# Optimization experiments

Hardware: AMD Instinct MI355X
Metric: run time of the kernel (lower is better)

The kernel has to match this reference:

```python
import jax, jax.numpy as jnp
import numpy as np

NUM_THETAS = 64   # bump_steps == num_thetas == 64
NUM_PTS = 100
B = 256           # number of graphs
N = B * NUM_PTS   # total nodes
SCALE = 500.0     # sigmoid sharpness used by EctLayer
HID = 4 * 1024


def _linear_init(key, fan_in, shape):
    s = 1.0 / np.sqrt(fan_in)
    return jax.random.uniform(key, shape, jnp.float32, -s, s)


def setup_inputs() -> dict:
    key = jax.random.key(0)
    ks = jax.random.split(key, 8)
    x = jax.random.normal(ks[0], (N, 2), jnp.float32)
    batch_idx = jnp.repeat(jnp.arange(B), NUM_PTS)  # [N] graph id per node
    t = jnp.linspace(0.0, 2.0 * np.pi, NUM_THETAS)
    V = jnp.stack([jnp.sin(t), jnp.cos(t)], axis=0)          # [2, T] directions
    lin = jnp.linspace(-1.0, 1.0, NUM_THETAS)                # [bump] thresholds
    d = NUM_THETAS * NUM_THETAS
    W1 = _linear_init(ks[1], d, (d, HID)); b1 = _linear_init(ks[2], d, (HID,))
    W2 = _linear_init(ks[3], HID, (HID, HID)); b2 = _linear_init(ks[4], HID, (HID,))
    W3 = _linear_init(ks[5], HID, (HID, 2 * NUM_PTS)); b3 = _linear_init(ks[6], HID, (2 * NUM_PTS,))
    return {"x": x, "batch_idx": batch_idx, "V": V, "lin": lin,
            "W1": W1, "b1": b1, "W2": W2, "b2": b2, "W3": W3, "b3": b3}


def ect_layer(x, idx, V, lin, num_graphs):
    # x: [N,2], V: [2,T] -> node heights nh: [N,T]
    nh = x @ V
    # soft-threshold binning: [N, bump, T]
    ecc = jax.nn.sigmoid(SCALE * (lin[None, :, None] - nh[:, None, :]))
    # per-graph scatter-sum over nodes -> [B, bump, T]
    e = jax.ops.segment_sum(ecc, idx, num_segments=num_graphs)
    # normalized=True: divide by per-graph max
    return e / jnp.amax(e, axis=(1, 2), keepdims=True)


def reference(x, batch_idx, V, lin, W1, b1, W2, b2, W3, b3):
    ect = ect_layer(x, batch_idx, V, lin, B)          # [B, 64, 64]
    h = ect.reshape(B, -1)                            # Flatten
    h = jnp.tanh(h @ W1 + b1)
    h = jnp.tanh(h @ W2 + b2)
    pts = (h @ W3 + b3).reshape(-1, 2)                # [B*NUM_PTS, 2]
    idx2 = jnp.repeat(jnp.arange(B), NUM_PTS)
    decoded = ect_layer(pts, idx2, V, lin, B)         # [B, 64, 64]
    return decoded, pts
```

## Files before the change

### kernel.cpp

```cpp
#include <hip/hip_runtime.h>
#include <hip/hip_bf16.h>

typedef short bf16x8 __attribute__((ext_vector_type(8)));
typedef short s16x4 __attribute__((ext_vector_type(4)));
typedef float f32x4 __attribute__((ext_vector_type(4)));
typedef unsigned u32x4 __attribute__((ext_vector_type(4)));

#define ECT_SCALE 500.0f

__device__ __forceinline__ bool detect_f32(const void* w) {
    const unsigned* p = (const unsigned*)w;
    int sane = 0;
#pragma unroll
    for (int i = 0; i < 16; i++) {
        unsigned e = (p[i] >> 7) & 0xFFu;
        sane += (e >= 100u && e <= 140u) ? 1 : 0;
    }
    return sane < 10;
}

__device__ __forceinline__ float ld_f(const void* p, int i, bool f32) {
    return f32 ? ((const float*)p)[i]
               : __bfloat162float(((const __hip_bfloat16*)p)[i]);
}

__device__ __forceinline__ void split_f(float v, short& hi, short& lo) {
    __hip_bfloat16 h = __float2bfloat16(v);
    hi = (short)__bfloat16_as_short(h);
    lo = (short)__bfloat16_as_short(__float2bfloat16(v - __bfloat162float(h)));
}

__device__ __forceinline__ float sig_fast(float x) {
    float t = __builtin_amdgcn_fmed3f(x, 0.0f, 1.0f);
    return t * t * (3.0f - 2.0f * t);
}

__global__ __launch_bounds__(512)
void ect1_kernel(const void* __restrict__ x, const void* __restrict__ V,
                 const void* __restrict__ lin, const void* __restrict__ sent,
                 short* __restrict__ eh, short* __restrict__ el)
{
    __shared__ float in_lds[200];
    __shared__ float nh[100 * 64];
    __shared__ float wmax[8];

    const bool f32 = detect_f32(sent);
    const int g = blockIdx.x, tid = threadIdx.x;
    const int t = tid & 63, wv = tid >> 6;

    if (tid < 200) in_lds[tid] = ld_f(x, g * 200 + tid, f32);
    const float sv = ld_f(V, t, f32);
    const float cv = ld_f(V, 64 + t, f32);
    float zs[8];
#pragma unroll
    for (int k = 0; k < 8; k++)
        zs[k] = (ECT_SCALE / 8.0f) * ld_f(lin, wv + 8 * k, f32) + 0.5f;
    __syncthreads();

    for (int n = wv; n < 100; n += 8)
        nh[n * 64 + t] = in_lds[2 * n] * sv + in_lds[2 * n + 1] * cv;

    float e[8];
#pragma unroll
    for (int k = 0; k < 8; k++) e[k] = 0.0f;
    __syncthreads();

    for (int n = 0; n < 100; n++) {
        const float ws = (ECT_SCALE / 8.0f) * nh[n * 64 + t];
#pragma unroll
        for (int k = 0; k < 8; k++)
            e[k] += sig_fast(zs[k] - ws);
    }

    float mx = e[0];
#pragma unroll
    for (int k = 1; k < 8; k++) mx = fmaxf(mx, e[k]);
#pragma unroll
    for (int off = 32; off > 0; off >>= 1)
        mx = fmaxf(mx, __shfl_xor(mx, off, 64));
    if (t == 0) wmax[wv] = mx;
    __syncthreads();
    float gm = wmax[0];
#pragma unroll
    for (int k = 1; k < 8; k++) gm = fmaxf(gm, wmax[k]);
    const float sc = 1.0f / gm;

#pragma unroll
    for (int k = 0; k < 8; k++) {
        short hi, lo;
        split_f(e[k] * sc, hi, lo);
        eh[g * 4096 + tid + 512 * k] = hi;
        el[g * 4096 + tid + 512 * k] = lo;
    }
}

#define GEMM_STAGE(K_, N_, GUARD_N)                                            \
    {                                                                          \
        _Pragma("unroll")                                                      \
        for (int i = 0; i < 2; i++) {                                          \
            int r = rr + 32 * i;                                               \
            *(bf16x8*)&Ahs[r][cc] =                                            \
                *(const bf16x8*)&Ah[(size_t)(bm * 64 + r) * K_ + k0 + cc];     \
            *(bf16x8*)&Als[r][cc] =                                            \
                *(const bf16x8*)&Al[(size_t)(bm * 64 + r) * K_ + k0 + cc];     \
        }                                                                      \
        {                                                                      \
            const int wn = lane;                                               \
            const int wk = wv * 16;                                            \
            const bool okn = !(GUARD_N) || (n0c + wn < N_);                    \
            unsigned hp[8], lp[8];                                             \
            if (f32) {                                                         \
                float w0[16];                                                  \
                _Pragma("unroll")                                              \
                for (int j = 0; j < 16; j++)                                   \
                    w0[j] = okn ? ((const float*)W)[(size_t)(k0 + wk + j) * N_ + n0c + wn] : 0.0f; \
                _Pragma("unroll")                                              \
                for (int jp = 0; jp < 8; jp++) {                               \
                    unsigned ua = __float_as_uint(w0[2 * jp]);                 \
                    unsigned ub = __float_as_uint(w0[2 * jp + 1]);             \
                    unsigned ha = ua & 0xFFFF0000u, hb = ub & 0xFFFF0000u;     \
                    hp[jp] = (ha >> 16) | hb;                                  \
                    float la = w0[2 * jp] - __uint_as_float(ha);               \
                    float lb = w0[2 * jp + 1] - __uint_as_float(hb);           \
                    lp[jp] = (__float_as_uint(la) >> 16) |                     \
                             (__float_as_uint(lb) & 0xFFFF0000u);              \
                }                                                              \
            } else {                                                           \
                unsigned short wu[16];                                         \
                _Pragma("unroll")                                              \
                for (int j = 0; j < 16; j++)                                   \
                    wu[j] = okn ? ((const unsigned short*)W)[(size_t)(k0 + wk + j) * N_ + n0c + wn] : (unsigned short)0; \
                _Pragma("unroll")                                              \
                for (int jp = 0; jp < 8; jp++) {                               \
                    hp[jp] = (unsigned)wu[2 * jp] | ((unsigned)wu[2 * jp + 1] << 16); \
                    lp[jp] = 0u;                                               \
                }                                                              \
            }                                                                  \
            *(u32x4*)&Bhs[wn][wk]     = (u32x4){hp[0], hp[1], hp[2], hp[3]};   \
            *(u32x4*)&Bhs[wn][wk + 8] = (u32x4){hp[4], hp[5], hp[6], hp[7]};   \
            *(u32x4*)&Bls[wn][wk]     = (u32x4){lp[0], lp[1], lp[2], lp[3]};   \
            *(u32x4*)&Bls[wn][wk + 8] = (u32x4){lp[4], lp[5], lp[6], lp[7]};   \
        }                                                                      \
        __syncthreads();                                                       \
        _Pragma("unroll")                                                      \
        for (int kh = 0; kh < 2; kh++) {                                       \
            bf16x8 ah[2], al[2], bh[2], bl[2];                                 \
            _Pragma("unroll")                                                  \
            for (int im = 0; im < 2; im++) {                                   \
                ah[im] = *(const bf16x8*)&Ahs[mrow0 + im * 16 + l16][kh * 32 + quad * 8]; \
                al[im] = *(const bf16x8*)&Als[mrow0 + im * 16 + l16][kh * 32 + quad * 8]; \
            }                                                                  \
            _Pragma("unroll")                                                  \
            for (int jn = 0; jn < 2; jn++) {                                   \
                bh[jn] = *(const bf16x8*)&Bhs[ncol0 + jn * 16 + l16][kh * 32 + quad * 8]; \
                bl[jn] = *(const bf16x8*)&Bls[ncol0 + jn * 16 + l16][kh * 32 + quad * 8]; \
            }                                                                  \
            _Pragma("unroll")                                                  \
            for (int im = 0; im < 2; im++)                                     \
                _Pragma("unroll")                                              \
                for (int jn = 0; jn < 2; jn++) {                               \
                    acc[im][jn] = __builtin_amdgcn_mfma_f32_16x16x32_bf16(ah[im], bh[jn], acc[im][jn], 0, 0, 0); \
                    acc[im][jn] = __builtin_amdgcn_mfma_f32_16x16x32_bf16(ah[im], bl[jn], acc[im][jn], 0, 0, 0); \
                    acc[im][jn] = __builtin_amdgcn_mfma_f32_16x16x32_bf16(al[im], bh[jn], acc[im][jn], 0, 0, 0); \
                }                                                              \
        }                                                                      \
        __syncthreads();                                                       \
    }

template<bool GUARD>
__global__ __launch_bounds__(256)
void gemm_sk(const short* __restrict__ Ah, const short* __restrict__ Al,
             const void* __restrict__ W, const void* __restrict__ sent,
             float* __restrict__ pre, int N_, int K_, int kzbits, int kiters)
{
    __shared__ short Ahs[64][72], Als[64][72], Bhs[64][72], Bls[64][72];
    const bool f32 = detect_f32(sent);
    const int bm = blockIdx.y;
    const int bn = blockIdx.x >> kzbits;
    const int kz = blockIdx.x & ((1 << kzbits) - 1);
    const int tid = threadIdx.x;
    const int wv = tid >> 6, lane = tid & 63, quad = lane >> 4, l16 = lane & 15;
    const int mrow0 = (wv & 1) * 32, ncol0 = (wv >> 1) * 32;
    const int rr = tid >> 3, cc = (tid & 7) * 8;
    const int n0c = bn * 64;

    f32x4 acc[2][2];
#pragma unroll
    for (int i = 0; i < 2; i++)
#pragma unroll
        for (int j = 0; j < 2; j++) acc[i][j] = (f32x4){0.f, 0.f, 0.f, 0.f};

    int k0 = kz * (kiters * 64);
    for (int it = 0; it < kiters; it++, k0 += 64)
        GEMM_STAGE(K_, N_, GUARD)

#pragma unroll
    for (int im = 0; im < 2; im++)
#pragma unroll
        for (int jn = 0; jn < 2; jn++) {
            const int n = n0c + ncol0 + jn * 16 + l16;
            if (!GUARD || n < N_) {
#pragma unroll
                for (int r = 0; r < 4; r++) {
                    const int m = bm * 64 + mrow0 + im * 16 + quad * 4 + r;
                    atomicAdd(&pre[(size_t)m * N_ + n], acc[im][jn][r]);
                }
            }
        }
}

__global__ __launch_bounds__(256)
void finalize_tanh(const float* __restrict__ pre, const void* __restrict__ bias,
                   const void* __restrict__ sent,
                   short* __restrict__ Oh, short* __restrict__ Ol)
{
    const bool f32 = detect_f32(sent);
    const int idx = (blockIdx.x * 256 + threadIdx.x) * 4;
    f32x4 v = *(const f32x4*)&pre[idx];
    const int n = idx & 4095;
    s16x4 hi, lo;
#pragma unroll
    for (int j = 0; j < 4; j++) {
        float t = v[j] + ld_f(bias, n + j, f32);
        t = 1.0f - 2.0f * __builtin_amdgcn_rcpf(1.0f + __expf(2.0f * t));
        short h, l;
        split_f(t, h, l);
        hi[j] = h; lo[j] = l;
    }
    *(s16x4*)&Oh[idx] = hi;
    *(s16x4*)&Ol[idx] = lo;
}

__global__ __launch_bounds__(512)
void ect2_kernel(const float* __restrict__ part, const void* __restrict__ bias3,
                 const void* __restrict__ V, const void* __restrict__ lin,
                 const void* __restrict__ sent,
                 float* __restrict__ dec, float* __restrict__ pts_out)
{
    __shared__ float in_lds[200];
    __shared__ float nh[100 * 64];
    __shared__ float wmax[8];

    const bool f32 = detect_f32(sent);
    const int g = blockIdx.x, tid = threadIdx.x;
    const int t = tid & 63, wv = tid >> 6;

    if (tid < 200) {
        float v = part[g * 200 + tid] + ld_f(bias3, tid, f32);
        in_lds[tid] = v;
        pts_out[g * 200 + tid] = v;
    }
    const float sv = ld_f(V, t, f32);
    const float cv = ld_f(V, 64 + t, f32);
    float zs[8];
#pragma unroll
    for (int k = 0; k < 8; k++)
        zs[k] = (ECT_SCALE / 8.0f) * ld_f(lin, wv + 8 * k, f32) + 0.5f;
    __syncthreads();

    for (int n = wv; n < 100; n += 8)
        nh[n * 64 + t] = in_lds[2 * n] * sv + in_lds[2 * n + 1] * cv;

    float e[8];
#pragma unroll
    for (int k = 0; k < 8; k++) e[k] = 0.0f;
    __syncthreads();

    for (int n = 0; n < 100; n++) {
        const float ws = (ECT_SCALE / 8.0f) * nh[n * 64 + t];
#pragma unroll
        for (int k = 0; k < 8; k++)
            e[k] += sig_fast(zs[k] - ws);
    }

    float mx = e[0];
#pragma unroll
    for (int k = 1; k < 8; k++) mx = fmaxf(mx, e[k]);
#pragma unroll
    for (int off = 32; off > 0; off >>= 1)
        mx = fmaxf(mx, __shfl_xor(mx, off, 64));
    if (t == 0) wmax[wv] = mx;
    __syncthreads();
    float gm = wmax[0];
#pragma unroll
    for (int k = 1; k < 8; k++) gm = fmaxf(gm, wmax[k]);
    const float sc = 1.0f / gm;

#pragma unroll
    for (int k = 0; k < 8; k++)
        dec[g * 4096 + tid + 512 * k] = e[k] * sc;
}

extern "C" void kernel_launch(void* const* d_in, const int* in_sizes, int n_in,
                              void* d_out, int out_size, void* d_ws, size_t ws_size,
                              hipStream_t stream)
{
    const void* x   = d_in[0];
    const void* V   = d_in[2];
    const void* lin = d_in[3];
    const void* W1  = d_in[4];
    const void* b1  = d_in[5];
    const void* W2  = d_in[6];
    const void* b2  = d_in[7];
    const void* W3  = d_in[8];
    const void* b3  = d_in[9];
    float* out = (float*)d_out;

    char* ws = (char*)d_ws;
    short* e_h  = (short*)(ws + ( 0u << 20));
    short* e_l  = (short*)(ws + ( 2u << 20));
    short* h1h  = (short*)(ws + ( 4u << 20));
    short* h1l  = (short*)(ws + ( 6u << 20));
    short* h2h  = (short*)(ws + ( 8u << 20));
    short* h2l  = (short*)(ws + (10u << 20));
    float* pre1 = (float*)(ws + (12u << 20));
    float* pre2 = (float*)(ws + (16u << 20));
    float* part = (float*)(ws + (20u << 20));

    hipMemsetAsync(ws + (12u << 20), 0, (8u << 20) + 256 * 200 * sizeof(float), stream);

    ect1_kernel<<<256, 512, 0, stream>>>(x, V, lin, W1, e_h, e_l);
    gemm_sk<false><<<dim3(256, 4), 256, 0, stream>>>(e_h, e_l, W1, W1, pre1, 4096, 4096, 2, 16);
    finalize_tanh<<<1024, 256, 0, stream>>>(pre1, b1, W1, h1h, h1l);
    gemm_sk<false><<<dim3(256, 4), 256, 0, stream>>>(h1h, h1l, W2, W1, pre2, 4096, 4096, 2, 16);
    finalize_tanh<<<1024, 256, 0, stream>>>(pre2, b2, W1, h2h, h2l);
    gemm_sk<true><<<dim3(128, 4), 256, 0, stream>>>(h2h, h2l, W3, W1, part, 200, 4096, 5, 2);
    ect2_kernel<<<256, 512, 0, stream>>>(part, b3, V, lin, W1, out, out + 1048576);
}
```

Baseline: 278.1 us.

## Use 128x128 tiles with register prefetch and deterministic split-K partial buffers

```diff
diff --git a/kernel.cpp b/kernel.cpp
--- a/kernel.cpp
+++ b/kernel.cpp
@@ -94,90 +94,149 @@
     }
 }
 
-#define GEMM_STAGE(K_, N_, GUARD_N)                                            \
+#define PREFETCH(k0_)                                                          \
     {                                                                          \
         _Pragma("unroll")                                                      \
-        for (int i = 0; i < 2; i++) {                                          \
-            int r = rr + 32 * i;                                               \
-            *(bf16x8*)&Ahs[r][cc] =                                            \
-                *(const bf16x8*)&Ah[(size_t)(bm * 64 + r) * K_ + k0 + cc];     \
-            *(bf16x8*)&Als[r][cc] =                                            \
-                *(const bf16x8*)&Al[(size_t)(bm * 64 + r) * K_ + k0 + cc];     \
+        for (int p = 0; p < 2; p++) {                                          \
+            int r = ar + 64 * p;                                               \
+            pah[p] = *(const bf16x8*)&Ah[(size_t)(bm * 128 + r) * 4096 + (k0_) + ac]; \
+            pal[p] = *(const bf16x8*)&Al[(size_t)(bm * 128 + r) * 4096 + (k0_) + ac]; \
         }                                                                      \
-        {                                                                      \
-            const int wn = lane;                                               \
-            const int wk = wv * 16;                                            \
-            const bool okn = !(GUARD_N) || (n0c + wn < N_);                    \
-            unsigned hp[8], lp[8];                                             \
-            if (f32) {                                                         \
-                float w0[16];                                                  \
-                _Pragma("unroll")                                              \
-                for (int j = 0; j < 16; j++)                                   \
-                    w0[j] = okn ? ((const float*)W)[(size_t)(k0 + wk + j) * N_ + n0c + wn] : 0.0f; \
-                _Pragma("unroll")                                              \
-                for (int jp = 0; jp < 8; jp++) {                               \
-                    unsigned ua = __float_as_uint(w0[2 * jp]);                 \
-                    unsigned ub = __float_as_uint(w0[2 * jp + 1]);             \
-                    unsigned ha = ua & 0xFFFF0000u, hb = ub & 0xFFFF0000u;     \
-                    hp[jp] = (ha >> 16) | hb;                                  \
-                    float la = w0[2 * jp] - __uint_as_float(ha);               \
-                    float lb = w0[2 * jp + 1] - __uint_as_float(hb);           \
-                    lp[jp] = (__float_as_uint(la) >> 16) |                     \
-                             (__float_as_uint(lb) & 0xFFFF0000u);              \
-                }                                                              \
-            } else {                                                           \
-                unsigned short wu[16];                                         \
-                _Pragma("unroll")                                              \
-                for (int j = 0; j < 16; j++)                                   \
-                    wu[j] = okn ? ((const unsigned short*)W)[(size_t)(k0 + wk + j) * N_ + n0c + wn] : (unsigned short)0; \
-                _Pragma("unroll")                                              \
-                for (int jp = 0; jp < 8; jp++) {                               \
-                    hp[jp] = (unsigned)wu[2 * jp] | ((unsigned)wu[2 * jp + 1] << 16); \
-                    lp[jp] = 0u;                                               \
-                }                                                              \
+        _Pragma("unroll")                                                      \
+        for (int c = 0; c < 2; c++)                                            \
+            _Pragma("unroll")                                                  \
+            for (int j = 0; j < 8; j++) {                                      \
+                size_t off = (size_t)((k0_) + wk + j) * 4096 + n0c + lane + 64 * c; \
+                pw[c * 8 + j] = f32 ? ((const unsigned*)W)[off]                \
+                                    : ((unsigned)((const unsigned short*)W)[off] << 16); \
             }                                                                  \
-            *(u32x4*)&Bhs[wn][wk]     = (u32x4){hp[0], hp[1], hp[2], hp[3]};   \
-            *(u32x4*)&Bhs[wn][wk + 8] = (u32x4){hp[4], hp[5], hp[6], hp[7]};   \
-            *(u32x4*)&Bls[wn][wk]     = (u32x4){lp[0], lp[1], lp[2], lp[3]};   \
-            *(u32x4*)&Bls[wn][wk + 8] = (u32x4){lp[4], lp[5], lp[6], lp[7]};   \
-        }                                                                      \
-        __syncthreads();                                                       \
-        _Pragma("unroll")                                                      \
-        for (int kh = 0; kh < 2; kh++) {                                       \
-            bf16x8 ah[2], al[2], bh[2], bl[2];                                 \
-            _Pragma("unroll")                                                  \
-            for (int im = 0; im < 2; im++) {                                   \
-                ah[im] = *(const bf16x8*)&Ahs[mrow0 + im * 16 + l16][kh * 32 + quad * 8]; \
-                al[im] = *(const bf16x8*)&Als[mrow0 + im * 16 + l16][kh * 32 + quad * 8]; \
-            }                                                                  \
-            _Pragma("unroll")                                                  \
-            for (int jn = 0; jn < 2; jn++) {                                   \
-                bh[jn] = *(const bf16x8*)&Bhs[ncol0 + jn * 16 + l16][kh * 32 + quad * 8]; \
-                bl[jn] = *(const bf16x8*)&Bls[ncol0 + jn * 16 + l16][kh * 32 + quad * 8]; \
-            }                                                                  \
-            _Pragma("unroll")                                                  \
-            for (int im = 0; im < 2; im++)                                     \
-                _Pragma("unroll")                                              \
-                for (int jn = 0; jn < 2; jn++) {                               \
-                    acc[im][jn] = __builtin_amdgcn_mfma_f32_16x16x32_bf16(ah[im], bh[jn], acc[im][jn], 0, 0, 0); \
-                    acc[im][jn] = __builtin_amdgcn_mfma_f32_16x16x32_bf16(ah[im], bl[jn], acc[im][jn], 0, 0, 0); \
-                    acc[im][jn] = __builtin_amdgcn_mfma_f32_16x16x32_bf16(al[im], bh[jn], acc[im][jn], 0, 0, 0); \
-                }                                                              \
-        }                                                                      \
-        __syncthreads();                                                       \
-    }
-
-template<bool GUARD>
+    }
+
 __global__ __launch_bounds__(256)
-void gemm_sk(const short* __restrict__ Ah, const short* __restrict__ Al,
+void gemm128(const short* __restrict__ Ah, const short* __restrict__ Al,
              const void* __restrict__ W, const void* __restrict__ sent,
-             float* __restrict__ pre, int N_, int K_, int kzbits, int kiters)
+             float* __restrict__ pre)
+{
+    __shared__ short Ahs[128][40], Als[128][40], Bhs[128][40], Bls[128][40];
+    const bool f32 = detect_f32(sent);
+    const int bm = blockIdx.y;
+    const int bn = blockIdx.x >> 3;
+    const int kz = blockIdx.x & 7;
+    const int tid = threadIdx.x;
+    const int wv = tid >> 6, lane = tid & 63, quad = lane >> 4, l16 = lane & 15;
+    const int wm = (wv & 1) * 64, wn = (wv >> 1) * 64;
+    const int ar = tid >> 2, ac = (tid & 3) * 8;
+    const int n0c = bn * 128;
+    const int wk = wv * 8;
+
+    f32x4 acc[4][4];
+#pragma unroll
+    for (int i = 0; i < 4; i++)
+#pragma unroll
+        for (int j = 0; j < 4; j++) acc[i][j] = (f32x4){0.f, 0.f, 0.f, 0.f};
+
+    bf16x8 pah[2], pal[2];
+    unsigned pw[16];
+
+    const int k0base = kz * 512;
+    PREFETCH(k0base)
+
+    for (int it = 0; it < 16; it++) {
+#pragma unroll
+        for (int p = 0; p < 2; p++) {
+            *(bf16x8*)&Ahs[ar + 64 * p][ac] = pah[p];
+            *(bf16x8*)&Als[ar + 64 * p][ac] = pal[p];
+        }
+#pragma unroll
+        for (int c = 0; c < 2; c++) {
+            unsigned hp[4], lp[4];
+#pragma unroll
+            for (int jp = 0; jp < 4; jp++) {
+                unsigned a = pw[c * 8 + 2 * jp], b = pw[c * 8 + 2 * jp + 1];
+                unsigned ha = a & 0xFFFF0000u, hb = b & 0xFFFF0000u;
+                hp[jp] = (ha >> 16) | hb;
+                float la = __uint_as_float(a) - __uint_as_float(ha);
+                float lb = __uint_as_float(b) - __uint_as_float(hb);
+                lp[jp] = (__float_as_uint(la) >> 16) |
+                         (__float_as_uint(lb) & 0xFFFF0000u);
+            }
+            *(u32x4*)&Bhs[lane + 64 * c][wk] = (u32x4){hp[0], hp[1], hp[2], hp[3]};
+            *(u32x4*)&Bls[lane + 64 * c][wk] = (u32x4){lp[0], lp[1], lp[2], lp[3]};
+        }
+        __syncthreads();
+
+        if (it < 15) PREFETCH(k0base + (it + 1) * 32)
+
+        bf16x8 ahf[4], alf[4];
+#pragma unroll
+        for (int i = 0; i < 4; i++) {
+            ahf[i] = *(const bf16x8*)&Ahs[wm + i * 16 + l16][quad * 8];
+            alf[i] = *(const bf16x8*)&Als[wm + i * 16 + l16][quad * 8];
+        }
+#pragma unroll
+        for (int j = 0; j < 4; j++) {
+            bf16x8 bh = *(const bf16x8*)&Bhs[wn + j * 16 + l16][quad * 8];
+            bf16x8 bl = *(const bf16x8*)&Bls[wn + j * 16 + l16][quad * 8];
+#pragma unroll
+            for (int i = 0; i < 4; i++) {
+                acc[i][j] = __builtin_amdgcn_mfma_f32_16x16x32_bf16(ahf[i], bh, acc[i][j], 0, 0, 0);
+                acc[i][j] = __builtin_amdgcn_mfma_f32_16x16x32_bf16(ahf[i], bl, acc[i][j], 0, 0, 0);
+                acc[i][j] = __builtin_amdgcn_mfma_f32_16x16x32_bf16(alf[i], bh, acc[i][j], 0, 0, 0);
+            }
+        }
+        __syncthreads();
+    }
+
+    float* ps = pre + (size_t)kz * (256 * 4096);
+#pragma unroll
+    for (int i = 0; i < 4; i++)
+#pragma unroll
+        for (int j = 0; j < 4; j++) {
+            const int n = n0c + wn + j * 16 + l16;
+#pragma unroll
+            for (int r = 0; r < 4; r++) {
+                const int m = bm * 128 + wm + i * 16 + quad * 4 + r;
+                ps[(size_t)m * 4096 + n] = acc[i][j][r];
+            }
+        }
+}
+
+__global__ __launch_bounds__(256)
+void finalize8(const float* __restrict__ pre, const void* __restrict__ bias,
+               const void* __restrict__ sent,
+               short* __restrict__ Oh, short* __restrict__ Ol)
+{
+    const bool f32 = detect_f32(sent);
+    const int idx = (blockIdx.x * 256 + threadIdx.x) * 4;
+    f32x4 s = (f32x4){0.f, 0.f, 0.f, 0.f};
+#pragma unroll
+    for (int z = 0; z < 8; z++)
+        s += *(const f32x4*)&pre[(size_t)z * 1048576 + idx];
+    const int n = idx & 4095;
+    s16x4 hi, lo;
+#pragma unroll
+    for (int j = 0; j < 4; j++) {
+        float t = s[j] + ld_f(bias, n + j, f32);
+        t = 1.0f - 2.0f * __builtin_amdgcn_rcpf(1.0f + __expf(2.0f * t));
+        short h, l;
+        split_f(t, h, l);
+        hi[j] = h; lo[j] = l;
+    }
+    *(s16x4*)&Oh[idx] = hi;
+    *(s16x4*)&Ol[idx] = lo;
+}
+
+__global__ __launch_bounds__(256)
+void gemm_sk3(const short* __restrict__ Ah, const short* __restrict__ Al,
+              const void* __restrict__ W, const void* __restrict__ sent,
+              float* __restrict__ part)
 {
     __shared__ short Ahs[64][72], Als[64][72], Bhs[64][72], Bls[64][72];
     const bool f32 = detect_f32(sent);
+    const int N_ = 200, K_ = 4096;
     const int bm = blockIdx.y;
-    const int bn = blockIdx.x >> kzbits;
-    const int kz = blockIdx.x & ((1 << kzbits) - 1);
+    const int bn = blockIdx.x >> 5;
+    const int kz = blockIdx.x & 31;
     const int tid = threadIdx.x;
     const int wv = tid >> 6, lane = tid & 63, quad = lane >> 4, l16 = lane & 15;
     const int mrow0 = (wv & 1) * 32, ncol0 = (wv >> 1) * 32;
@@ -190,45 +249,78 @@
 #pragma unroll
         for (int j = 0; j < 2; j++) acc[i][j] = (f32x4){0.f, 0.f, 0.f, 0.f};
 
-    int k0 = kz * (kiters * 64);
-    for (int it = 0; it < kiters; it++, k0 += 64)
-        GEMM_STAGE(K_, N_, GUARD)
-
+    int k0 = kz * 128;
+    for (int it = 0; it < 2; it++, k0 += 64) {
+#pragma unroll
+        for (int i = 0; i < 2; i++) {
+            int r = rr + 32 * i;
+            *(bf16x8*)&Ahs[r][cc] = *(const bf16x8*)&Ah[(size_t)(bm * 64 + r) * K_ + k0 + cc];
+            *(bf16x8*)&Als[r][cc] = *(const bf16x8*)&Al[(size_t)(bm * 64 + r) * K_ + k0 + cc];
+        }
+        {
+            const int wn2 = lane, wk2 = wv * 16;
+            const bool okn = (n0c + wn2 < N_);
+            unsigned pw2[16];
+#pragma unroll
+            for (int j = 0; j < 16; j++) {
+                size_t off = (size_t)(k0 + wk2 + j) * N_ + n0c + wn2;
+                pw2[j] = !okn ? 0u
+                       : (f32 ? ((const unsigned*)W)[off]
+                              : ((unsigned)((const unsigned short*)W)[off] << 16));
+            }
+            unsigned hp[8], lp[8];
+#pragma unroll
+            for (int jp = 0; jp < 8; jp++) {
+                unsigned a = pw2[2 * jp], b = pw2[2 * jp + 1];
+                unsigned ha = a & 0xFFFF0000u, hb = b & 0xFFFF0000u;
+                hp[jp] = (ha >> 16) | hb;
+                float la = __uint_as_float(a) - __uint_as_float(ha);
+                float lb = __uint_as_float(b) - __uint_as_float(hb);
+                lp[jp] = (__float_as_uint(la) >> 16) | (__float_as_uint(lb) & 0xFFFF0000u);
+            }
+            *(u32x4*)&Bhs[wn2][wk2]     = (u32x4){hp[0], hp[1], hp[2], hp[3]};
+            *(u32x4*)&Bhs[wn2][wk2 + 8] = (u32x4){hp[4], hp[5], hp[6], hp[7]};
+            *(u32x4*)&Bls[wn2][wk2]     = (u32x4){lp[0], lp[1], lp[2], lp[3]};
+            *(u32x4*)&Bls[wn2][wk2 + 8] = (u32x4){lp[4], lp[5], lp[6], lp[7]};
+        }
+        __syncthreads();
+#pragma unroll
+        for (int kh = 0; kh < 2; kh++) {
+            bf16x8 ah2[2], al2[2];
+#pragma unroll
+            for (int im = 0; im < 2; im++) {
+                ah2[im] = *(const bf16x8*)&Ahs[mrow0 + im * 16 + l16][kh * 32 + quad * 8];
+                al2[im] = *(const bf16x8*)&Als[mrow0 + im * 16 + l16][kh * 32 + quad * 8];
+            }
+#pragma unroll
+            for (int jn = 0; jn < 2; jn++) {
+                bf16x8 bh = *(const bf16x8*)&Bhs[ncol0 + jn * 16 + l16][kh * 32 + quad * 8];
+                bf16x8 bl = *(const bf16x8*)&Bls[ncol0 + jn * 16 + l16][kh * 32 + quad * 8];
+#pragma unroll
+                for (int im = 0; im < 2; im++) {
+                    acc[im][jn] = __builtin_amdgcn_mfma_f32_16x16x32_bf16(ah2[im], bh, acc[im][jn], 0, 0, 0);
+                    acc[im][jn] = __builtin_amdgcn_mfma_f32_16x16x32_bf16(ah2[im], bl, acc[im][jn], 0, 0, 0);
+                    acc[im][jn] = __builtin_amdgcn_mfma_f32_16x16x32_bf16(al2[im], bh, acc[im][jn], 0, 0, 0);
+                }
+            }
+        }
+        __syncthreads();
+    }
+
+    float* ps = part + (size_t)kz * (256 * 200);
 #pragma unroll
     for (int im = 0; im < 2; im++)
 #pragma unroll
         for (int jn = 0; jn < 2; jn++) {
             const int n = n0c + ncol0 + jn * 16 + l16;
-            if (!GUARD || n < N_) {
+            if (n < N_) {
 #pragma unroll
                 for (int r = 0; r < 4; r++) {
                     const int m = bm * 64 + mrow0 + im * 16 + quad * 4 + r;
-                    atomicAdd(&pre[(size_t)m * N_ + n], acc[im][jn][r]);
+                    ps[m * 200 + n] = acc[im][jn][r];
                 }
             }
         }
-}
-
-__global__ __launch_bounds__(256)
-void finalize_tanh(const float* __restrict__ pre, const void* __restrict__ bias,
-                   const void* __restrict__ sent,
-                   short* __restrict__ Oh, short* __restrict__ Ol)
-{
-    const bool f32 = detect_f32(sent);
-    const int idx = (blockIdx.x * 256 + threadIdx.x) * 4;
-    f32x4 v = *(const f32x4*)&pre[idx];
-    const int n = idx & 4095;
-    s16x4 hi, lo;
-#pragma unroll
-    for (int j = 0; j < 4; j++) {
-        float t = v[j] + ld_f(bias, n + j, f32);
-        t = 1.0f - 2.0f * __builtin_amdgcn_rcpf(1.0f + __expf(2.0f * t));
-        short h, l;
-        split_f(t, h, l);
-        hi[j] = h; lo[j] = l;
-    }
-    *(s16x4*)&Oh[idx] = hi;
-    *(s16x4*)&Ol[idx] = lo;
 }
 
 __global__ __launch_bounds__(512)
@@ -246,7 +338,10 @@
     const int t = tid & 63, wv = tid >> 6;
 
     if (tid < 200) {
-        float v = part[g * 200 + tid] + ld_f(bias3, tid, f32);
+        float v = ld_f(bias3, tid, f32);
+#pragma unroll
+        for (int z = 0; z < 32; z++)
+            v += part[(size_t)z * 51200 + g * 200 + tid];
         in_lds[tid] = v;
         pts_out[g * 200 + tid] = v;
     }
@@ -313,17 +408,14 @@
     short* h1l  = (short*)(ws + ( 6u << 20));
     short* h2h  = (short*)(ws + ( 8u << 20));
     short* h2l  = (short*)(ws + (10u << 20));
-    float* pre1 = (float*)(ws + (12u << 20));
-    float* pre2 = (float*)(ws + (16u << 20));
-    float* part = (float*)(ws + (20u << 20));
-
-    hipMemsetAsync(ws + (12u << 20), 0, (8u << 20) + 256 * 200 * sizeof(float), stream);
+    float* pre  = (float*)(ws + (12u << 20));
+    float* part = (float*)(ws + (44u << 20));
 
     ect1_kernel<<<256, 512, 0, stream>>>(x, V, lin, W1, e_h, e_l);
-    gemm_sk<false><<<dim3(256, 4), 256, 0, stream>>>(e_h, e_l, W1, W1, pre1, 4096, 4096, 2, 16);
-    finalize_tanh<<<1024, 256, 0, stream>>>(pre1, b1, W1, h1h, h1l);
-    gemm_sk<false><<<dim3(256, 4), 256, 0, stream>>>(h1h, h1l, W2, W1, pre2, 4096, 4096, 2, 16);
-    finalize_tanh<<<1024, 256, 0, stream>>>(pre2, b2, W1, h2h, h2l);
-    gemm_sk<true><<<dim3(128, 4), 256, 0, stream>>>(h2h, h2l, W3, W1, part, 200, 4096, 5, 2);
+    gemm128<<<dim3(256, 2), 256, 0, stream>>>(e_h, e_l, W1, W1, pre);
+    finalize8<<<1024, 256, 0, stream>>>(pre, b1, W1, h1h, h1l);
+    gemm128<<<dim3(256, 2), 256, 0, stream>>>(h1h, h1l, W2, W1, pre);
+    finalize8<<<1024, 256, 0, stream>>>(pre, b2, W1, h2h, h2l);
+    gemm_sk3<<<dim3(128, 4), 256, 0, stream>>>(h2h, h2l, W3, W1, part);
     ect2_kernel<<<256, 512, 0, stream>>>(part, b3, V, lin, W1, out, out + 1048576);
 }
```

Measured after the change: 271.7 us. -2.3%, faster.
